# Kernel optimization log

Measured on AMD Instinct MI355X. Metric: run time of the kernel, lower is better.

The kernel has to match this reference:

```python
import jax, jax.numpy as jnp
import numpy as np

B, H, W = 8, 56, 56
DIM = 384
NH = 8
HD = DIM // NH          # 48, also the depthwise-conv channel count
WS = 14
HID = 4 * DIM           # mlp hidden
EPS = 1e-5              # torch nn.LayerNorm default
SCALE = HD ** -0.5


def ln(x, w, b):
    m = jnp.mean(x, axis=-1, keepdims=True)
    v = jnp.var(x, axis=-1, keepdims=True)
    return (x - m) * jax.lax.rsqrt(v + EPS) * w + b


def dwconv3x3(x, w):
    # x: [N,H,W,C], w: [3,3,1,C] depthwise (groups=C), stride 1, pad 1, no bias
    return jax.lax.conv_general_dilated(
        x, w, window_strides=(1, 1), padding=((1, 1), (1, 1)),
        dimension_numbers=('NHWC', 'HWIO', 'NHWC'),
        feature_group_count=x.shape[-1])


def rel_table(rel_pos, size):
    # rel_pos: [2*size-1, HD] -> [size, size, HD] via relative coords (stride 1, q==k size)
    idx = jnp.arange(size)[:, None] - jnp.arange(size)[None, :] + (size - 1)
    return rel_pos[idx]


def win_part(x, ws):
    # [N,H,W,C] -> [N*nWh*nWw, ws, ws, C]  (H,W divisible by ws here)
    N, Hh, Ww, C = x.shape
    x = x.reshape(N, Hh // ws, ws, Ww // ws, ws, C)
    return x.transpose(0, 1, 3, 2, 4, 5).reshape(-1, ws, ws, C)


def win_unpart(x, ws, Hh, Ww):
    nW = (Hh // ws) * (Ww // ws)
    N = x.shape[0] // nW
    x = x.reshape(N, Hh // ws, Ww // ws, ws, ws, -1)
    return x.transpose(0, 1, 3, 2, 4, 5).reshape(N, Hh, Ww, -1)


def _forward(x1, x2, norm1_w, norm1_b, qkv_w, qkv_b,
             poolq_w, poolk_w, poolv_w,
             nq_w, nq_b, nk_w, nk_b, nv_w, nv_b,
             rel_h, rel_w, proj_w, proj_b,
             norm2_w, norm2_b, fc1_w, fc1_b, fc2_w, fc2_b):
    # ---- F(x1): MultiScaleAttention(norm1(x1)) ----
    xn = ln(x1, norm1_w, norm1_b)
    qkv = (xn @ qkv_w + qkv_b).reshape(B, H, W, 3, NH, HD)
    qkv = qkv.transpose(3, 0, 4, 1, 2, 5).reshape(3, B * NH, H, W, HD)
    q = ln(dwconv3x3(qkv[0], poolq_w), nq_w, nq_b)
    k = ln(dwconv3x3(qkv[1], poolk_w), nk_w, nk_b)
    v = ln(dwconv3x3(qkv[2], poolv_w), nv_w, nv_b)
    ori_q = q
    qw = win_part(q, WS).reshape(-1, WS * WS, HD)   # [Bw, 196, 48]
    kw = win_part(k, WS).reshape(-1, WS * WS, HD)
    vw = win_part(v, WS).reshape(-1, WS * WS, HD)
    attn = jnp.einsum('bqc,bkc->bqk', qw * SCALE, kw)
    # decomposed relative position bias
    Rh = rel_table(rel_h, WS)                       # [14,14,48]
    Rw = rel_table(rel_w, WS)
    rq = qw.reshape(-1, WS, WS, HD)
    bh = jnp.einsum('bhwc,hkc->bhwk', rq, Rh)
    bw = jnp.einsum('bhwc,wkc->bhwk', rq, Rw)
    attn = (attn.reshape(-1, WS, WS, WS, WS)
            + bh[:, :, :, :, None] + bw[:, :, :, None, :]).reshape(-1, WS * WS, WS * WS)
    attn = jax.nn.softmax(attn, axis=-1)
    o = jnp.einsum('bqk,bkc->bqc', attn, vw).reshape(-1, WS, WS, HD)
    o = win_unpart(o, WS, H, W)
    o = o + ori_q                                    # residual pooling
    o = o.reshape(B, NH, H, W, HD).transpose(0, 2, 3, 1, 4).reshape(B, H, W, DIM)
    f = o @ proj_w + proj_b
    y1 = x1 + f
    # ---- G(y1): Mlp(norm2(y1)) ----
    yn = ln(y1, norm2_w, norm2_b)
    g = jax.nn.gelu(yn @ fc1_w + fc1_b, approximate=False) @ fc2_w + fc2_b
    y2 = x2 + g
    return y1, y2


def setup_inputs() -> dict:
    key = jax.random.key(0)
    ks = jax.random.split(key, 32)
    p = lambda i, shape, s: jax.random.normal(ks[i], shape, jnp.float32) * s
    return {
        'x1': jax.random.normal(ks[0], (B, H, W, DIM), jnp.float32),
        'x2': jax.random.normal(ks[1], (B, H, W, DIM), jnp.float32),
        'norm1_w': jnp.ones((DIM,), jnp.float32),
        'norm1_b': jnp.zeros((DIM,), jnp.float32),
        'qkv_w': p(2, (DIM, 3 * DIM), 0.02),
        'qkv_b': jnp.zeros((3 * DIM,), jnp.float32),
        'poolq_w': p(3, (3, 3, 1, HD), 0.1),
        'poolk_w': p(4, (3, 3, 1, HD), 0.1),
        'poolv_w': p(5, (3, 3, 1, HD), 0.1),
        'nq_w': jnp.ones((HD,), jnp.float32), 'nq_b': jnp.zeros((HD,), jnp.float32),
        'nk_w': jnp.ones((HD,), jnp.float32), 'nk_b': jnp.zeros((HD,), jnp.float32),
        'nv_w': jnp.ones((HD,), jnp.float32), 'nv_b': jnp.zeros((HD,), jnp.float32),
        'rel_h': p(6, (2 * WS - 1, HD), 0.02),
        'rel_w': p(7, (2 * WS - 1, HD), 0.02),
        'proj_w': p(8, (DIM, DIM), 0.02),
        'proj_b': jnp.zeros((DIM,), jnp.float32),
        'norm2_w': jnp.ones((DIM,), jnp.float32),
        'norm2_b': jnp.zeros((DIM,), jnp.float32),
        'fc1_w': p(9, (DIM, HID), 0.02),
        'fc1_b': jnp.zeros((HID,), jnp.float32),
        'fc2_w': p(10, (HID, DIM), 0.02),
        'fc2_b': jnp.zeros((DIM,), jnp.float32),
    }


def reference(x1, x2, norm1_w, norm1_b, qkv_w, qkv_b,
              poolq_w, poolk_w, poolv_w,
              nq_w, nq_b, nk_w, nk_b, nv_w, nv_b,
              rel_h, rel_w, proj_w, proj_b,
              norm2_w, norm2_b, fc1_w, fc1_b, fc2_w, fc2_b):
    return _forward(x1, x2, norm1_w, norm1_b, qkv_w, qkv_b,
                    poolq_w, poolk_w, poolv_w,
                    nq_w, nq_b, nk_w, nk_b, nv_w, nv_b,
                    rel_h, rel_w, proj_w, proj_b,
                    norm2_w, norm2_b, fc1_w, fc1_b, fc2_w, fc2_b)
```

## Files before the change

kernel.cpp:

```cpp
#include <hip/hip_runtime.h>
#include <hip/hip_bf16.h>

typedef unsigned short u16;
typedef unsigned int u32;

#define DEVI __device__ __forceinline__

constexpr int BB = 8, HHc = 56, WWc = 56, DIMC = 384, NHC = 8, HDC = 48, WSZ = 14;
constexpr int NTOK = BB * HHc * WWc;
constexpr int HIDC = 4 * DIMC;
constexpr float EPSF = 1e-5f;
constexpr float SCALEF = 0.14433756729740643f;

typedef short bf16x8 __attribute__((ext_vector_type(8)));
typedef float f32x4 __attribute__((ext_vector_type(4)));

DEVI float b2f(u16 u) { u32 x = ((u32)u) << 16; float f; __builtin_memcpy(&f, &x, 4); return f; }
DEVI float uasf(u32 x) { float f; __builtin_memcpy(&f, &x, 4); return f; }
DEVI u16 f2b(float f) {
  u32 x; __builtin_memcpy(&x, &f, 4);
  u32 r = (x >> 16) & 1u; x += 0x7fffu + r;
  return (u16)(x >> 16);
}

DEVI float wred_sum(float v) {
  #pragma unroll
  for (int o = 32; o; o >>= 1) v += __shfl_xor(v, o);
  return v;
}

#define GLOAD_LDS16(g, l) __builtin_amdgcn_global_load_lds( \
    (const __attribute__((address_space(1))) u32*)(g), \
    (__attribute__((address_space(3))) u32*)(l), 16, 0, 0)

__global__ __launch_bounds__(256)
void wcvt_kernel(const float* __restrict__ in, u16* __restrict__ out, int K, int N) {
  __shared__ float t[32][33];
  int bk = blockIdx.x * 32, bn = blockIdx.y * 32;
  int tx = threadIdx.x & 31, ty = threadIdx.x >> 5;
  #pragma unroll
  for (int i = 0; i < 32; i += 8)
    t[ty + i][tx] = in[(size_t)(bk + ty + i) * N + bn + tx];
  __syncthreads();
  #pragma unroll
  for (int i = 0; i < 32; i += 8)
    out[(size_t)(bn + ty + i) * K + bk + tx] = f2b(t[tx][ty + i]);
}

__global__ __launch_bounds__(256)
void ln384_kernel(const float* __restrict__ x, const float* __restrict__ w,
                  const float* __restrict__ b, u16* __restrict__ out) {
  int wave = threadIdx.x >> 6, lane = threadIdx.x & 63;
  int tok = blockIdx.x * 4 + wave;
  if (tok >= NTOK) return;
  const float* xr = x + (size_t)tok * DIMC;
  float v[6]; float s = 0.f, ss = 0.f;
  #pragma unroll
  for (int i = 0; i < 6; ++i) {
    v[i] = xr[lane + i * 64];
    s += v[i]; ss += v[i] * v[i];
  }
  s = wred_sum(s); ss = wred_sum(ss);
  float mean = s * (1.f / 384.f);
  float var = ss * (1.f / 384.f) - mean * mean;
  float inv = rsqrtf(var + EPSF);
  #pragma unroll
  for (int i = 0; i < 6; ++i) {
    int c = lane + i * 64;
    out[(size_t)(c >> 5) * (NTOK * 32) + (size_t)tok * 32 + (c & 31)] =
        f2b((v[i] - mean) * inv * w[c] + b[c]);
  }
}

template<int MODE>
__global__ __launch_bounds__(256)
void mgemm_kernel(const u16* __restrict__ A, const u16* __restrict__ Wt,
                  const float* __restrict__ bias, const float* __restrict__ res,
                  void* __restrict__ outv, int M, int N, int K) {
  __shared__ __attribute__((aligned(16))) u16 As[3][128 * 32];
  __shared__ __attribute__((aligned(16))) u16 Bs[3][128 * 32];
  int tid = threadIdx.x;
  int wave = tid >> 6, lane = tid & 63;
  int wr = wave >> 1, wc = wave & 1;
  int bm0 = blockIdx.x * 128, bn0 = blockIdx.y * 128;
  int lrow = lane >> 2;
  int slot = (lane & 3) ^ ((lane >> 3) & 3);
  const size_t slab = (size_t)M * 32;
  const u16* ag0 = A + (size_t)(bm0 + wave * 32 + lrow) * 32 + slot * 8;
  const u16* ag1 = ag0 + 16 * 32;
  const u16* bg0 = Wt + (size_t)(bn0 + wave * 32 + lrow) * K + slot * 8;
  const u16* bg1 = bg0 + (size_t)16 * K;
  int q4 = lane >> 4, r16 = lane & 15;
  int rslot = (q4 ^ ((r16 >> 1) & 3)) * 8;
  int aoff = (wr * 64 + r16) * 32 + rslot;
  int boff = (wc * 64 + r16) * 32 + rslot;
  f32x4 acc[4][4] = {};
  int nk = K >> 5;
  {
    u16* a0 = As[0] + wave * 1024; u16* b0 = Bs[0] + wave * 1024;
    GLOAD_LDS16(ag0, a0);              GLOAD_LDS16(ag1, a0 + 512);
    GLOAD_LDS16(bg0, b0);              GLOAD_LDS16(bg1, b0 + 512);
    u16* a1 = As[1] + wave * 1024; u16* b1 = Bs[1] + wave * 1024;
    GLOAD_LDS16(ag0 + slab, a1);       GLOAD_LDS16(ag1 + slab, a1 + 512);
    GLOAD_LDS16(bg0 + 32, b1);         GLOAD_LDS16(bg1 + 32, b1 + 512);
  }
  int cur = 0, pf = 2;
  for (int t = 0; t < nk; ++t) {
    if (t + 2 < nk) {
      int k0 = (t + 2) << 5;
      u16* a0 = As[pf] + wave * 1024; u16* b0 = Bs[pf] + wave * 1024;
      GLOAD_LDS16(ag0 + (size_t)(t + 2) * slab, a0);
      GLOAD_LDS16(ag1 + (size_t)(t + 2) * slab, a0 + 512);
      GLOAD_LDS16(bg0 + k0, b0);  GLOAD_LDS16(bg1 + k0, b0 + 512);
      asm volatile("s_waitcnt vmcnt(8)" ::: "memory");
    } else if (t + 1 < nk) {
      asm volatile("s_waitcnt vmcnt(4)" ::: "memory");
    } else {
      asm volatile("s_waitcnt vmcnt(0)" ::: "memory");
    }
    __builtin_amdgcn_s_barrier();
    const u16* ar = As[cur] + aoff;
    const u16* br = Bs[cur] + boff;
    bf16x8 af[4], bf[4];
    #pragma unroll
    for (int f = 0; f < 4; ++f) {
      af[f] = *reinterpret_cast<const bf16x8*>(ar + f * 512);
      bf[f] = *reinterpret_cast<const bf16x8*>(br + f * 512);
    }
    #pragma unroll
    for (int fm = 0; fm < 4; ++fm)
      #pragma unroll
      for (int fn = 0; fn < 4; ++fn)
        acc[fm][fn] = __builtin_amdgcn_mfma_f32_16x16x32_bf16(af[fm], bf[fn], acc[fm][fn], 0, 0, 0);
    asm volatile("s_waitcnt lgkmcnt(0)" ::: "memory");
    __builtin_amdgcn_s_barrier();
    cur = (cur == 2) ? 0 : cur + 1;
    pf  = (pf  == 2) ? 0 : pf  + 1;
  }
  int c0 = bn0 + wc * 64 + r16;
  int r0 = bm0 + wr * 64 + q4 * 4;
  #pragma unroll
  for (int fm = 0; fm < 4; ++fm) {
    #pragma unroll
    for (int fn = 0; fn < 4; ++fn) {
      int c = c0 + fn * 16;
      float bsv = bias[c];
      #pragma unroll
      for (int j = 0; j < 4; ++j) {
        int r = r0 + fm * 16 + j;
        float v = acc[fm][fn][j] + bsv;
        if constexpr (MODE == 0) {
          u16* out = (u16*)outv;
          int s = c / DIMC; int rem = c - s * DIMC;
          int nh = rem / HDC; int ch = rem - nh * HDC;
          int b = r / 3136; int hw = r - b * 3136;
          out[(((size_t)(s * 64 + b * 8 + nh)) * 3136 + hw) * 48 + ch] = f2b(v);
        } else if constexpr (MODE == 1) {
          float* out = (float*)outv;
          size_t idx = (size_t)r * N + c;
          out[idx] = v + res[idx];
        } else {
          u16* out = (u16*)outv;
          out[(size_t)(c >> 5) * M * 32 + (size_t)r * 32 + (c & 31)] =
              f2b(0.5f * v * (1.0f + erff(v * 0.70710678118654752440f)));
        }
      }
    }
  }
}

__global__ __launch_bounds__(256)
void convln_kernel(const u16* __restrict__ qkv,
                   const float* __restrict__ wq, const float* __restrict__ wk, const float* __restrict__ wv,
                   const float* __restrict__ gq, const float* __restrict__ bq,
                   const float* __restrict__ gk, const float* __restrict__ bk,
                   const float* __restrict__ gv, const float* __restrict__ bv,
                   u16* __restrict__ out) {
  __shared__ __attribute__((aligned(16))) float wsm[432];
  __shared__ __attribute__((aligned(16))) float gsm[48];
  __shared__ __attribute__((aligned(16))) float bsm[48];
  int tid = threadIdx.x;
  int sb = blockIdx.y;
  int s = sb >> 6;
  const float* wgt = (s == 0) ? wq : ((s == 1) ? wk : wv);
  const float* gam = (s == 0) ? gq : ((s == 1) ? gk : gv);
  const float* bet = (s == 0) ? bq : ((s == 1) ? bk : bv);
  for (int i = tid; i < 432; i += 256) wsm[i] = wgt[i];
  if (tid < 48) { gsm[tid] = gam[tid]; bsm[tid] = bet[tid]; }
  __syncthreads();
  int hw = blockIdx.x * 256 + tid;
  if (hw >= 3136) return;
  int h = hw / 56, w = hw - h * 56;
  const u16* img = qkv + (size_t)sb * (3136 * 48);
  float acc[48];
  #pragma unroll
  for (int c = 0; c < 48; ++c) acc[c] = 0.f;
  #pragma unroll
  for (int dy = -1; dy <= 1; ++dy) {
    int hh = h + dy;
    if ((unsigned)hh >= 56u) continue;
    #pragma unroll
    for (int dx = -1; dx <= 1; ++dx) {
      int ww = w + dx;
      if ((unsigned)ww >= 56u) continue;
      const uint4* p = reinterpret_cast<const uint4*>(img + (size_t)(hh * 56 + ww) * 48);
      const float4* wr = reinterpret_cast<const float4*>(wsm + ((dy + 1) * 3 + (dx + 1)) * 48);
      #pragma unroll
      for (int g = 0; g < 6; ++g) {
        uint4 v = p[g];
        float4 w0 = wr[g * 2], w1 = wr[g * 2 + 1];
        acc[g * 8 + 0] += uasf(v.x << 16)          * w0.x;
        acc[g * 8 + 1] += uasf(v.x & 0xFFFF0000u)  * w0.y;
        acc[g * 8 + 2] += uasf(v.y << 16)          * w0.z;
        acc[g * 8 + 3] += uasf(v.y & 0xFFFF0000u)  * w0.w;
        acc[g * 8 + 4] += uasf(v.z << 16)          * w1.x;
        acc[g * 8 + 5] += uasf(v.z & 0xFFFF0000u)  * w1.y;
        acc[g * 8 + 6] += uasf(v.w << 16)          * w1.z;
        acc[g * 8 + 7] += uasf(v.w & 0xFFFF0000u)  * w1.w;
      }
    }
  }
  float sum = 0.f, ssq = 0.f;
  #pragma unroll
  for (int c = 0; c < 48; ++c) { sum += acc[c]; ssq += acc[c] * acc[c]; }
  float mean = sum * (1.f / 48.f);
  float var = ssq * (1.f / 48.f) - mean * mean;
  float inv = rsqrtf(var + EPSF);
  u16* op = out + ((size_t)sb * 3136 + hw) * 48;
  #pragma unroll
  for (int g = 0; g < 6; ++g) {
    const float4 gm0 = *reinterpret_cast<const float4*>(gsm + g * 8);
    const float4 gm1 = *reinterpret_cast<const float4*>(gsm + g * 8 + 4);
    const float4 bt0 = *reinterpret_cast<const float4*>(bsm + g * 8);
    const float4 bt1 = *reinterpret_cast<const float4*>(bsm + g * 8 + 4);
    uint4 ov;
    u32 a0 = f2b((acc[g * 8 + 0] - mean) * inv * gm0.x + bt0.x);
    u32 a1 = f2b((acc[g * 8 + 1] - mean) * inv * gm0.y + bt0.y);
    u32 a2 = f2b((acc[g * 8 + 2] - mean) * inv * gm0.z + bt0.z);
    u32 a3 = f2b((acc[g * 8 + 3] - mean) * inv * gm0.w + bt0.w);
    u32 a4 = f2b((acc[g * 8 + 4] - mean) * inv * gm1.x + bt1.x);
    u32 a5 = f2b((acc[g * 8 + 5] - mean) * inv * gm1.y + bt1.y);
    u32 a6 = f2b((acc[g * 8 + 6] - mean) * inv * gm1.z + bt1.z);
    u32 a7 = f2b((acc[g * 8 + 7] - mean) * inv * gm1.w + bt1.w);
    ov.x = a0 | (a1 << 16);
    ov.y = a2 | (a3 << 16);
    ov.z = a4 | (a5 << 16);
    ov.w = a6 | (a7 << 16);
    *reinterpret_cast<uint4*>(op + g * 8) = ov;
  }
}

#define MFMA16(a, b, c) __builtin_amdgcn_mfma_f32_16x16x32_bf16((a), (b), (c), 0, 0, 0)
constexpr int LDP = 224;
constexpr int LDK = 104;
constexpr int LDV = 228;
__global__ __launch_bounds__(512, 1)
void attn_kernel(const u16* __restrict__ qkvc, const float* __restrict__ rel_h,
                 const float* __restrict__ rel_w, u16* __restrict__ obuf) {
  __shared__ __attribute__((aligned(16))) u16 KL[208 * LDK];
  __shared__ __attribute__((aligned(16))) u16 VT[48 * LDV];
  __shared__ __attribute__((aligned(16))) u16 QE[208 * 56];
  __shared__ __attribute__((aligned(16))) u16 PB[8 * 16 * LDP];

  int wid = blockIdx.x;
  int bnh = wid >> 4, wrem = wid & 15, wh = wrem >> 2, wwn = wrem & 3;
  int tid = threadIdx.x;
  int wave = tid >> 6, lane = tid & 63;
  int q4 = lane >> 4, r16 = lane & 15;

  { u32* z;
    z = (u32*)KL; for (int i = tid; i < 208 * LDK / 2; i += 512) z[i] = 0;
    z = (u32*)VT; for (int i = tid; i < 48 * LDV / 2; i += 512) z[i] = 0;
    z = (u32*)PB; for (int i = tid; i < 64 * 72 / 2; i += 512) z[i] = 0;
  }
  __syncthreads();
  size_t qbase = (size_t)bnh * 3136 * 48;
  size_t kbase = ((size_t)(64 + bnh) * 3136) * 48;
  size_t vbase = ((size_t)(128 + bnh) * 3136) * 48;
  for (int i = tid; i < 196 * 12; i += 512) {
    int r = i / 12, c4 = (i - r * 12) * 4;
    int h = wh * 14 + r / 14, w = wwn * 14 + r % 14;
    size_t g = (size_t)(h * 56 + w) * 48 + c4;
    ushort4 kv = *reinterpret_cast<const ushort4*>(qkvc + kbase + g);
    kv.x = f2b(b2f(kv.x) * SCALEF); kv.y = f2b(b2f(kv.y) * SCALEF);
    kv.z = f2b(b2f(kv.z) * SCALEF); kv.w = f2b(b2f(kv.w) * SCALEF);
    *reinterpret_cast<ushort4*>(KL + r * LDK + c4) = kv;
    ushort4 vv = *reinterpret_cast<const ushort4*>(qkvc + vbase + g);
    VT[(c4 + 0) * LDV + r] = vv.x; VT[(c4 + 1) * LDV + r] = vv.y;
    VT[(c4 + 2) * LDV + r] = vv.z; VT[(c4 + 3) * LDV + r] = vv.w;
  }
  for (int r = tid; r < 208; r += 512) {
    if (r < 196) {
      KL[r * LDK + 48 + r / 14] = 0x3F80;
      KL[r * LDK + 62 + r % 14] = 0x3F80;
    } else {
      KL[r * LDK + 76] = 0x3F80;
    }
  }
  for (int i = tid; i < 54 * 48; i += 512) {
    int r = i / 48, c = i - r * 48;
    float v = (r < 27) ? rel_h[r * 48 + c] : rel_w[(r - 27) * 48 + c];
    PB[r * 72 + c] = f2b(v);
  }
  __syncthreads();
  for (int mf = wave; mf < 13; mf += 8) {
    int qrow = mf * 16 + r16; int qc = qrow < 196 ? qrow : 195;
    int hq = wh * 14 + qc / 14, wq = wwn * 14 + qc % 14;
    const u16* qpg = qkvc + qbase + (size_t)(hq * 56 + wq) * 48;
    bf16x8 af0 = *reinterpret_cast<const bf16x8*>(qpg + q4 * 8);
    bf16x8 af1 = {0, 0, 0, 0, 0, 0, 0, 0};
    if (q4 < 2) af1 = *reinterpret_cast<const bf16x8*>(qpg + 32 + q4 * 8);
    #pragma unroll
    for (int nf = 0; nf < 4; ++nf) {
      bf16x8 b0 = *reinterpret_cast<const bf16x8*>(PB + (nf * 16 + r16) * 72 + q4 * 8);
      bf16x8 b1 = *reinterpret_cast<const bf16x8*>(PB + (nf * 16 + r16) * 72 + 32 + q4 * 8);
      f32x4 acc = {};
      acc = MFMA16(af0, b0, acc);
      acc = MFMA16(af1, b1, acc);
      int col = nf * 16 + r16;
      if (col < 54) {
        #pragma unroll
        for (int j = 0; j < 4; ++j)
          QE[(mf * 16 + q4 * 4 + j) * 56 + col] = f2b(acc[j]);
      }
    }
  }
  __syncthreads();
  u16 bhv[14], bwv[14];
  {
    int t = tid;
    if (t < 208) {
      int qc = t < 196 ? t : 195;
      int qh = qc / 14, qw = qc - qh * 14;
      const u16* src = QE + t * 56;
      #pragma unroll
      for (int z = 0; z < 14; ++z) {
        bhv[z] = src[qh + 13 - z];
        bwv[z] = src[27 + qw + 13 - z];
      }
    }
  }
  __syncthreads();
  {
    int t = tid;
    if (t < 208) {
      u16* dst = QE + t * 56;
      #pragma unroll
      for (int z = 0; z < 14; ++z) { dst[z] = bhv[z]; dst[14 + z] = bwv[z]; }
      dst[28] = f2b(-30000.0f);
      #pragma unroll
      for (int z = 29; z < 56; ++z) dst[z] = 0;
    }
  }
  u16* Pw = PB + wave * 16 * LDP;
  for (int i = lane; i < 16 * 16; i += 64) {
    int r = i >> 4;
    Pw[r * LDP + ((208 + (i & 15)) ^ (((r >> 2) & 3) << 3))] = 0;
  }
  __syncthreads();
  int bI = bnh >> 3, nhI = bnh & 7;
  for (int mf = wave; mf < 13; mf += 8) {
    int qrow = mf * 16 + r16; int qc = qrow < 196 ? qrow : 195;
    int hq = wh * 14 + qc / 14, wq = wwn * 14 + qc % 14;
    const u16* qpg = qkvc + qbase + (size_t)(hq * 56 + wq) * 48;
    const u16* qe = QE + qrow * 56;
    bf16x8 af0 = *reinterpret_cast<const bf16x8*>(qpg + q4 * 8);
    bf16x8 af1;
    if (q4 < 2) af1 = *reinterpret_cast<const bf16x8*>(qpg + 32 + q4 * 8);
    else        af1 = *reinterpret_cast<const bf16x8*>(qe + (q4 - 2) * 8);
    bf16x8 af2 = *reinterpret_cast<const bf16x8*>(qe + 16 + q4 * 8);
    f32x4 s[13];
    #pragma unroll
    for (int nf = 0; nf < 13; ++nf) {
      const u16* kr = KL + (nf * 16 + r16) * LDK;
      bf16x8 b0 = *reinterpret_cast<const bf16x8*>(kr + q4 * 8);
      bf16x8 b1 = *reinterpret_cast<const bf16x8*>(kr + 32 + q4 * 8);
      bf16x8 b2 = *reinterpret_cast<const bf16x8*>(kr + 64 + q4 * 8);
      f32x4 a = {};
      a = MFMA16(af0, b0, a);
      a = MFMA16(af1, b1, a);
      a = MFMA16(af2, b2, a);
      s[nf] = a;
    }
    int rowb = mf * 16 + q4 * 4;
    float mrow[4], den[4];
    #pragma unroll
    for (int j = 0; j < 4; ++j) {
      float mm = s[0][j];
      #pragma unroll
      for (int nf = 1; nf < 13; ++nf) mm = fmaxf(mm, s[nf][j]);
      #pragma unroll
      for (int off = 1; off < 16; off <<= 1) mm = fmaxf(mm, __shfl_xor(mm, off));
      mrow[j] = mm; den[j] = 0.f;
    }
    #pragma unroll
    for (int nf = 0; nf < 13; ++nf) {
      #pragma unroll
      for (int j = 0; j < 4; ++j) {
        float p = __expf(s[nf][j] - mrow[j]);
        den[j] += p;
        Pw[(q4 * 4 + j) * LDP + (((nf * 16 + r16) ^ (q4 << 3)))] = f2b(p);
      }
    }
    #pragma unroll
    for (int j = 0; j < 4; ++j)
      #pragma unroll
      for (int off = 1; off < 16; off <<= 1) den[j] += __shfl_xor(den[j], off);
    f32x4 o[3] = {};
    #pragma unroll
    for (int ks = 0; ks < 7; ++ks) {
      bf16x8 ap = *reinterpret_cast<const bf16x8*>(
          Pw + r16 * LDP + ((ks * 32 + q4 * 8) ^ (((r16 >> 2) & 3) << 3)));
      #pragma unroll
      for (int nf3 = 0; nf3 < 3; ++nf3) {
        bf16x8 bv = *reinterpret_cast<const bf16x8*>(VT + (nf3 * 16 + r16) * LDV + ks * 32 + q4 * 8);
        o[nf3] = MFMA16(ap, bv, o[nf3]);
      }
    }
    #pragma unroll
    for (int j = 0; j < 4; ++j) {
      int row = rowb + j;
      if (row < 196) {
        float rden = 1.f / den[j];
        int rh = row / 14;
        int h = wh * 14 + rh, w = wwn * 14 + row - rh * 14;
        int tok = (bI * 56 + h) * 56 + w;
        const u16* qg = qkvc + qbase + (size_t)(h * 56 + w) * 48;
        #pragma unroll
        for (int nf3 = 0; nf3 < 3; ++nf3) {
          int col = nf3 * 16 + r16;
          int cg = nhI * 48 + col;
          obuf[(size_t)(cg >> 5) * (NTOK * 32) + (size_t)tok * 32 + (cg & 31)] =
              f2b(o[nf3][j] * rden + b2f(qg[col]));
        }
      }
    }
  }
}

extern "C" void kernel_launch(void* const* d_in, const int* in_sizes, int n_in,
                              void* d_out, int out_size, void* d_ws, size_t ws_size,
                              hipStream_t stream) {
  const float* x1      = (const float*)d_in[0];
  const float* x2      = (const float*)d_in[1];
  const float* norm1_w = (const float*)d_in[2];
  const float* norm1_b = (const float*)d_in[3];
  const float* qkv_w   = (const float*)d_in[4];
  const float* qkv_b   = (const float*)d_in[5];
  const float* poolq_w = (const float*)d_in[6];
  const float* poolk_w = (const float*)d_in[7];
  const float* poolv_w = (const float*)d_in[8];
  const float* nq_w    = (const float*)d_in[9];
  const float* nq_b    = (const float*)d_in[10];
  const float* nk_w    = (const float*)d_in[11];
  const float* nk_b    = (const float*)d_in[12];
  const float* nv_w    = (const float*)d_in[13];
  const float* nv_b    = (const float*)d_in[14];
  const float* rel_h   = (const float*)d_in[15];
  const float* rel_w   = (const float*)d_in[16];
  const float* proj_w  = (const float*)d_in[17];
  const float* proj_b  = (const float*)d_in[18];
  const float* norm2_w = (const float*)d_in[19];
  const float* norm2_b = (const float*)d_in[20];
  const float* fc1_w   = (const float*)d_in[21];
  const float* fc1_b   = (const float*)d_in[22];
  const float* fc2_w   = (const float*)d_in[23];
  const float* fc2_b   = (const float*)d_in[24];

  u16* ws      = (u16*)d_ws;
  u16* qkv     = ws;
  u16* xn      = ws + 28901376;
  u16* qkvc    = ws + 28901376;
  u16* obuf    = ws;
  u16* h1      = ws;
  u16* yn      = ws + 48168960;
  u16* qkv_wt  = ws + 38535168;
  u16* proj_wt = ws + 9633792;
  u16* fc1_wt  = ws + 38535168;
  u16* fc2_wt  = ws + 39124992;
  float* y1 = (float*)d_out;
  float* y2 = y1 + 9633792;

  wcvt_kernel<<<dim3(12, 36), 256, 0, stream>>>(qkv_w, qkv_wt, 384, 1152);
  ln384_kernel<<<NTOK / 4, 256, 0, stream>>>(x1, norm1_w, norm1_b, xn);
  mgemm_kernel<0><<<dim3(196, 9), 256, 0, stream>>>(xn, qkv_wt, qkv_b, nullptr, qkv, NTOK, 1152, 384);
  convln_kernel<<<dim3(13, 192), 256, 0, stream>>>(qkv, poolq_w, poolk_w, poolv_w,
                                                   nq_w, nq_b, nk_w, nk_b, nv_w, nv_b, qkvc);
  wcvt_kernel<<<dim3(12, 12), 256, 0, stream>>>(proj_w, proj_wt, 384, 384);
  attn_kernel<<<1024, 512, 0, stream>>>(qkvc, rel_h, rel_w, obuf);
  wcvt_kernel<<<dim3(12, 48), 256, 0, stream>>>(fc1_w, fc1_wt, 384, 1536);
  wcvt_kernel<<<dim3(48, 12), 256, 0, stream>>>(fc2_w, fc2_wt, 1536, 384);
  mgemm_kernel<1><<<dim3(196, 3), 256, 0, stream>>>(obuf, proj_wt, proj_b, x1, y1, NTOK, 384, 384);
  ln384_kernel<<<NTOK / 4, 256, 0, stream>>>(y1, norm2_w, norm2_b, yn);
  mgemm_kernel<2><<<dim3(196, 12), 256, 0, stream>>>(yn, fc1_wt, fc1_b, nullptr, h1, NTOK, 1536, 384);
  mgemm_kernel<1><<<dim3(196, 3), 256, 0, stream>>>(h1, fc2_wt, fc2_b, x2, y2, NTOK, 384, 1536);
}
```

Before: 372.4 us.

## Template GEMM on N tile width and switch to double-buffered LDS pipeline

Adds a BN template parameter so the two N=384 GEMMs (proj, fc2) use 128x64 tiles with twice as many blocks, improving occupancy and CU coverage for the smaller output. It also replaces the triple-buffered, two-ahead prefetch with a double-buffered, one-ahead prefetch, cutting LDS use per block. The trade-off is less prefetch depth, which may expose more global load latency, and a lower MFMA-to-load ratio in the 64-wide variant.

```diff
diff --git a/kernel.cpp b/kernel.cpp
--- a/kernel.cpp
+++ b/kernel.cpp
@@ -72,77 +72,78 @@
   }
 }
 
-template<int MODE>
+template<int MODE, int BN>
 __global__ __launch_bounds__(256)
 void mgemm_kernel(const u16* __restrict__ A, const u16* __restrict__ Wt,
                   const float* __restrict__ bias, const float* __restrict__ res,
                   void* __restrict__ outv, int M, int N, int K) {
-  __shared__ __attribute__((aligned(16))) u16 As[3][128 * 32];
-  __shared__ __attribute__((aligned(16))) u16 Bs[3][128 * 32];
+  constexpr int FN = BN / 32;
+  __shared__ __attribute__((aligned(16))) u16 As[2][128 * 32];
+  __shared__ __attribute__((aligned(16))) u16 Bs[2][BN * 32];
   int tid = threadIdx.x;
   int wave = tid >> 6, lane = tid & 63;
   int wr = wave >> 1, wc = wave & 1;
-  int bm0 = blockIdx.x * 128, bn0 = blockIdx.y * 128;
+  int bm0 = blockIdx.x * 128, bn0 = blockIdx.y * BN;
   int lrow = lane >> 2;
   int slot = (lane & 3) ^ ((lane >> 3) & 3);
   const size_t slab = (size_t)M * 32;
   const u16* ag0 = A + (size_t)(bm0 + wave * 32 + lrow) * 32 + slot * 8;
   const u16* ag1 = ag0 + 16 * 32;
-  const u16* bg0 = Wt + (size_t)(bn0 + wave * 32 + lrow) * K + slot * 8;
+  const u16* bg0 = Wt + (size_t)(bn0 + wave * (BN / 4) + lrow) * K + slot * 8;
   const u16* bg1 = bg0 + (size_t)16 * K;
   int q4 = lane >> 4, r16 = lane & 15;
   int rslot = (q4 ^ ((r16 >> 1) & 3)) * 8;
   int aoff = (wr * 64 + r16) * 32 + rslot;
-  int boff = (wc * 64 + r16) * 32 + rslot;
-  f32x4 acc[4][4] = {};
+  int boff = (wc * (BN / 2) + r16) * 32 + rslot;
+  f32x4 acc[4][FN] = {};
   int nk = K >> 5;
   {
-    u16* a0 = As[0] + wave * 1024; u16* b0 = Bs[0] + wave * 1024;
-    GLOAD_LDS16(ag0, a0);              GLOAD_LDS16(ag1, a0 + 512);
-    GLOAD_LDS16(bg0, b0);              GLOAD_LDS16(bg1, b0 + 512);
-    u16* a1 = As[1] + wave * 1024; u16* b1 = Bs[1] + wave * 1024;
-    GLOAD_LDS16(ag0 + slab, a1);       GLOAD_LDS16(ag1 + slab, a1 + 512);
-    GLOAD_LDS16(bg0 + 32, b1);         GLOAD_LDS16(bg1 + 32, b1 + 512);
-  }
-  int cur = 0, pf = 2;
+    u16* a0 = As[0] + wave * 1024;
+    u16* b0 = Bs[0] + wave * (BN / 4) * 32;
+    GLOAD_LDS16(ag0, a0);  GLOAD_LDS16(ag1, a0 + 512);
+    GLOAD_LDS16(bg0, b0);
+    if constexpr (BN == 128) GLOAD_LDS16(bg1, b0 + 512);
+  }
+  int cur = 0;
   for (int t = 0; t < nk; ++t) {
-    if (t + 2 < nk) {
-      int k0 = (t + 2) << 5;
-      u16* a0 = As[pf] + wave * 1024; u16* b0 = Bs[pf] + wave * 1024;
-      GLOAD_LDS16(ag0 + (size_t)(t + 2) * slab, a0);
-      GLOAD_LDS16(ag1 + (size_t)(t + 2) * slab, a0 + 512);
-      GLOAD_LDS16(bg0 + k0, b0);  GLOAD_LDS16(bg1 + k0, b0 + 512);
-      asm volatile("s_waitcnt vmcnt(8)" ::: "memory");
-    } else if (t + 1 < nk) {
-      asm volatile("s_waitcnt vmcnt(4)" ::: "memory");
+    if (t + 1 < nk) {
+      int k0 = (t + 1) << 5;
+      u16* a0 = As[cur ^ 1] + wave * 1024;
+      u16* b0 = Bs[cur ^ 1] + wave * (BN / 4) * 32;
+      GLOAD_LDS16(ag0 + (size_t)(t + 1) * slab, a0);
+      GLOAD_LDS16(ag1 + (size_t)(t + 1) * slab, a0 + 512);
+      GLOAD_LDS16(bg0 + k0, b0);
+      if constexpr (BN == 128) GLOAD_LDS16(bg1 + k0, b0 + 512);
+      if constexpr (BN == 128) asm volatile("s_waitcnt vmcnt(4)" ::: "memory");
+      else                     asm volatile("s_waitcnt vmcnt(3)" ::: "memory");
     } else {
       asm volatile("s_waitcnt vmcnt(0)" ::: "memory");
     }
     __builtin_amdgcn_s_barrier();
     const u16* ar = As[cur] + aoff;
     const u16* br = Bs[cur] + boff;
-    bf16x8 af[4], bf[4];
-    #pragma unroll
-    for (int f = 0; f < 4; ++f) {
+    bf16x8 af[4], bf[FN];
+    #pragma unroll
+    for (int f = 0; f < 4; ++f)
       af[f] = *reinterpret_cast<const bf16x8*>(ar + f * 512);
+    #pragma unroll
+    for (int f = 0; f < FN; ++f)
       bf[f] = *reinterpret_cast<const bf16x8*>(br + f * 512);
-    }
     #pragma unroll
     for (int fm = 0; fm < 4; ++fm)
       #pragma unroll
-      for (int fn = 0; fn < 4; ++fn)
+      for (int fn = 0; fn < FN; ++fn)
         acc[fm][fn] = __builtin_amdgcn_mfma_f32_16x16x32_bf16(af[fm], bf[fn], acc[fm][fn], 0, 0, 0);
     asm volatile("s_waitcnt lgkmcnt(0)" ::: "memory");
     __builtin_amdgcn_s_barrier();
-    cur = (cur == 2) ? 0 : cur + 1;
-    pf  = (pf  == 2) ? 0 : pf  + 1;
-  }
-  int c0 = bn0 + wc * 64 + r16;
+    cur ^= 1;
+  }
+  int c0 = bn0 + wc * (BN / 2) + r16;
   int r0 = bm0 + wr * 64 + q4 * 4;
   #pragma unroll
   for (int fm = 0; fm < 4; ++fm) {
     #pragma unroll
-    for (int fn = 0; fn < 4; ++fn) {
+    for (int fn = 0; fn < FN; ++fn) {
       int c = c0 + fn * 16;
       float bsv = bias[c];
       #pragma unroll
@@ -483,15 +484,15 @@
 
   wcvt_kernel<<<dim3(12, 36), 256, 0, stream>>>(qkv_w, qkv_wt, 384, 1152);
   ln384_kernel<<<NTOK / 4, 256, 0, stream>>>(x1, norm1_w, norm1_b, xn);
-  mgemm_kernel<0><<<dim3(196, 9), 256, 0, stream>>>(xn, qkv_wt, qkv_b, nullptr, qkv, NTOK, 1152, 384);
+  mgemm_kernel<0, 128><<<dim3(196, 9), 256, 0, stream>>>(xn, qkv_wt, qkv_b, nullptr, qkv, NTOK, 1152, 384);
   convln_kernel<<<dim3(13, 192), 256, 0, stream>>>(qkv, poolq_w, poolk_w, poolv_w,
                                                    nq_w, nq_b, nk_w, nk_b, nv_w, nv_b, qkvc);
   wcvt_kernel<<<dim3(12, 12), 256, 0, stream>>>(proj_w, proj_wt, 384, 384);
   attn_kernel<<<1024, 512, 0, stream>>>(qkvc, rel_h, rel_w, obuf);
   wcvt_kernel<<<dim3(12, 48), 256, 0, stream>>>(fc1_w, fc1_wt, 384, 1536);
   wcvt_kernel<<<dim3(48, 12), 256, 0, stream>>>(fc2_w, fc2_wt, 1536, 384);
-  mgemm_kernel<1><<<dim3(196, 3), 256, 0, stream>>>(obuf, proj_wt, proj_b, x1, y1, NTOK, 384, 384);
+  mgemm_kernel<1, 64><<<dim3(196, 6), 256, 0, stream>>>(obuf, proj_wt, proj_b, x1, y1, NTOK, 384, 384);
   ln384_kernel<<<NTOK / 4, 256, 0, stream>>>(y1, norm2_w, norm2_b, yn);
-  mgemm_kernel<2><<<dim3(196, 12), 256, 0, stream>>>(yn, fc1_wt, fc1_b, nullptr, h1, NTOK, 1536, 384);
-  mgemm_kernel<1><<<dim3(196, 3), 256, 0, stream>>>(h1, fc2_wt, fc2_b, x2, y2, NTOK, 384, 1536);
-}
+  mgemm_kernel<2, 128><<<dim3(196, 12), 256, 0, stream>>>(yn, fc1_wt, fc1_b, nullptr, h1, NTOK, 1536, 384);
+  mgemm_kernel<1, 64><<<dim3(196, 6), 256, 0, stream>>>(h1, fc2_wt, fc2_b, x2, y2, NTOK, 384, 1536);
+}
```

Result: faster. 361.4 us (-3.0%).

## Replace 4-wave 128x128 GEMM with single-wave 64x64 GEMM, B in registers

Applied to the files above, without the earlier changes.

Replaces the 256-thread 128x128-tile GEMM with a 64-thread single-wave kernel that computes a 64x64 tile. Only A is staged in LDS, through a 4-deep async ring. B fragments are loaded straight from global memory into double-buffered registers. This removes the block-level barriers and the B LDS traffic, and launches far more, smaller blocks for load balancing. The cost is less data reuse per tile: each A and B element is fetched from global/L2 more often, and direct global B loads may add latency.

```diff
diff --git a/kernel.cpp b/kernel.cpp
--- a/kernel.cpp
+++ b/kernel.cpp
@@ -32,6 +32,8 @@
 #define GLOAD_LDS16(g, l) __builtin_amdgcn_global_load_lds( \
     (const __attribute__((address_space(1))) u32*)(g), \
     (__attribute__((address_space(3))) u32*)(l), 16, 0, 0)
+
+#define MFMA16(a, b, c) __builtin_amdgcn_mfma_f32_16x16x32_bf16((a), (b), (c), 0, 0, 0)
 
 __global__ __launch_bounds__(256)
 void wcvt_kernel(const float* __restrict__ in, u16* __restrict__ out, int K, int N) {
@@ -73,81 +75,76 @@
 }
 
 template<int MODE>
-__global__ __launch_bounds__(256)
-void mgemm_kernel(const u16* __restrict__ A, const u16* __restrict__ Wt,
+__global__ __launch_bounds__(64)
+void wgemm_kernel(const u16* __restrict__ A, const u16* __restrict__ Wt,
                   const float* __restrict__ bias, const float* __restrict__ res,
                   void* __restrict__ outv, int M, int N, int K) {
-  __shared__ __attribute__((aligned(16))) u16 As[3][128 * 32];
-  __shared__ __attribute__((aligned(16))) u16 Bs[3][128 * 32];
-  int tid = threadIdx.x;
-  int wave = tid >> 6, lane = tid & 63;
-  int wr = wave >> 1, wc = wave & 1;
-  int bm0 = blockIdx.x * 128, bn0 = blockIdx.y * 128;
+  __shared__ __attribute__((aligned(16))) u16 As[4][64 * 32];
+  int lane = threadIdx.x;
+  int q4 = lane >> 4, r16 = lane & 15;
+  int bm0 = blockIdx.y * 64, bn0 = blockIdx.x * 64;
   int lrow = lane >> 2;
   int slot = (lane & 3) ^ ((lane >> 3) & 3);
   const size_t slab = (size_t)M * 32;
-  const u16* ag0 = A + (size_t)(bm0 + wave * 32 + lrow) * 32 + slot * 8;
-  const u16* ag1 = ag0 + 16 * 32;
-  const u16* bg0 = Wt + (size_t)(bn0 + wave * 32 + lrow) * K + slot * 8;
-  const u16* bg1 = bg0 + (size_t)16 * K;
-  int q4 = lane >> 4, r16 = lane & 15;
+  const u16* ag = A + (size_t)(bm0 + lrow) * 32 + slot * 8;
+  const u16* bg = Wt + (size_t)(bn0 + r16) * K + q4 * 8;
   int rslot = (q4 ^ ((r16 >> 1) & 3)) * 8;
-  int aoff = (wr * 64 + r16) * 32 + rslot;
-  int boff = (wc * 64 + r16) * 32 + rslot;
+  const int aoff = r16 * 32 + rslot;
   f32x4 acc[4][4] = {};
   int nk = K >> 5;
-  {
-    u16* a0 = As[0] + wave * 1024; u16* b0 = Bs[0] + wave * 1024;
-    GLOAD_LDS16(ag0, a0);              GLOAD_LDS16(ag1, a0 + 512);
-    GLOAD_LDS16(bg0, b0);              GLOAD_LDS16(bg1, b0 + 512);
-    u16* a1 = As[1] + wave * 1024; u16* b1 = Bs[1] + wave * 1024;
-    GLOAD_LDS16(ag0 + slab, a1);       GLOAD_LDS16(ag1 + slab, a1 + 512);
-    GLOAD_LDS16(bg0 + 32, b1);         GLOAD_LDS16(bg1 + 32, b1 + 512);
-  }
-  int cur = 0, pf = 2;
-  for (int t = 0; t < nk; ++t) {
-    if (t + 2 < nk) {
-      int k0 = (t + 2) << 5;
-      u16* a0 = As[pf] + wave * 1024; u16* b0 = Bs[pf] + wave * 1024;
-      GLOAD_LDS16(ag0 + (size_t)(t + 2) * slab, a0);
-      GLOAD_LDS16(ag1 + (size_t)(t + 2) * slab, a0 + 512);
-      GLOAD_LDS16(bg0 + k0, b0);  GLOAD_LDS16(bg1 + k0, b0 + 512);
-      asm volatile("s_waitcnt vmcnt(8)" ::: "memory");
-    } else if (t + 1 < nk) {
-      asm volatile("s_waitcnt vmcnt(4)" ::: "memory");
-    } else {
-      asm volatile("s_waitcnt vmcnt(0)" ::: "memory");
-    }
-    __builtin_amdgcn_s_barrier();
-    const u16* ar = As[cur] + aoff;
-    const u16* br = Bs[cur] + boff;
-    bf16x8 af[4], bf[4];
-    #pragma unroll
-    for (int f = 0; f < 4; ++f) {
-      af[f] = *reinterpret_cast<const bf16x8*>(ar + f * 512);
-      bf[f] = *reinterpret_cast<const bf16x8*>(br + f * 512);
-    }
-    #pragma unroll
-    for (int fm = 0; fm < 4; ++fm)
-      #pragma unroll
-      for (int fn = 0; fn < 4; ++fn)
-        acc[fm][fn] = __builtin_amdgcn_mfma_f32_16x16x32_bf16(af[fm], bf[fn], acc[fm][fn], 0, 0, 0);
-    asm volatile("s_waitcnt lgkmcnt(0)" ::: "memory");
-    __builtin_amdgcn_s_barrier();
-    cur = (cur == 2) ? 0 : cur + 1;
-    pf  = (pf  == 2) ? 0 : pf  + 1;
-  }
-  int c0 = bn0 + wc * 64 + r16;
-  int r0 = bm0 + wr * 64 + q4 * 4;
+  bf16x8 bA[4], bB[4];
+  #pragma unroll
+  for (int fn = 0; fn < 4; ++fn)
+    bA[fn] = *reinterpret_cast<const bf16x8*>(bg + (size_t)fn * 16 * K);
+  #pragma unroll
+  for (int i = 0; i < 3; ++i)
+    #pragma unroll
+    for (int r = 0; r < 4; ++r)
+      GLOAD_LDS16(ag + (size_t)i * slab + r * 16 * 32, As[i] + r * 16 * 32);
+
+#define WG_STEP(TT, BU, BL)                                                    \
+  {                                                                            \
+    int tt = (TT);                                                             \
+    if (tt + 1 < nk) {                                                         \
+      _Pragma("unroll")                                                        \
+      for (int fn = 0; fn < 4; ++fn)                                           \
+        BL[fn] = *reinterpret_cast<const bf16x8*>(                             \
+            bg + (size_t)fn * 16 * K + (tt + 1) * 32);                         \
+    }                                                                          \
+    if (tt + 3 < nk) {                                                         \
+      _Pragma("unroll")                                                        \
+      for (int r = 0; r < 4; ++r)                                              \
+        GLOAD_LDS16(ag + (size_t)(tt + 3) * slab + r * 16 * 32,                \
+                    As[(tt + 3) & 3] + r * 16 * 32);                           \
+      asm volatile("s_waitcnt vmcnt(12)" ::: "memory");                        \
+    } else {                                                                   \
+      asm volatile("s_waitcnt vmcnt(0)" ::: "memory");                         \
+    }                                                                          \
+    const u16* ar = As[tt & 3] + aoff;                                         \
+    _Pragma("unroll")                                                          \
+    for (int fm = 0; fm < 4; ++fm) {                                           \
+      bf16x8 af = *reinterpret_cast<const bf16x8*>(ar + fm * 16 * 32);         \
+      _Pragma("unroll")                                                        \
+      for (int fn = 0; fn < 4; ++fn)                                           \
+        acc[fm][fn] = MFMA16(af, BU[fn], acc[fm][fn]);                         \
+    }                                                                          \
+    asm volatile("s_waitcnt lgkmcnt(0)" ::: "memory");                         \
+  }
+
+  for (int t = 0; t < nk; t += 2) {
+    WG_STEP(t,     bA, bB);
+    WG_STEP(t + 1, bB, bA);
+  }
+#undef WG_STEP
   #pragma unroll
   for (int fm = 0; fm < 4; ++fm) {
     #pragma unroll
     for (int fn = 0; fn < 4; ++fn) {
-      int c = c0 + fn * 16;
+      int c = bn0 + fn * 16 + r16;
       float bsv = bias[c];
       #pragma unroll
       for (int j = 0; j < 4; ++j) {
-        int r = r0 + fm * 16 + j;
+        int r = bm0 + fm * 16 + q4 * 4 + j;
         float v = acc[fm][fn][j] + bsv;
         if constexpr (MODE == 0) {
           u16* out = (u16*)outv;
@@ -250,7 +247,6 @@
   }
 }
 
-#define MFMA16(a, b, c) __builtin_amdgcn_mfma_f32_16x16x32_bf16((a), (b), (c), 0, 0, 0)
 constexpr int LDP = 224;
 constexpr int LDK = 104;
 constexpr int LDV = 228;
@@ -483,15 +479,15 @@
 
   wcvt_kernel<<<dim3(12, 36), 256, 0, stream>>>(qkv_w, qkv_wt, 384, 1152);
   ln384_kernel<<<NTOK / 4, 256, 0, stream>>>(x1, norm1_w, norm1_b, xn);
-  mgemm_kernel<0><<<dim3(196, 9), 256, 0, stream>>>(xn, qkv_wt, qkv_b, nullptr, qkv, NTOK, 1152, 384);
+  wgemm_kernel<0><<<dim3(18, 392), 64, 0, stream>>>(xn, qkv_wt, qkv_b, nullptr, qkv, NTOK, 1152, 384);
   convln_kernel<<<dim3(13, 192), 256, 0, stream>>>(qkv, poolq_w, poolk_w, poolv_w,
                                                    nq_w, nq_b, nk_w, nk_b, nv_w, nv_b, qkvc);
   wcvt_kernel<<<dim3(12, 12), 256, 0, stream>>>(proj_w, proj_wt, 384, 384);
   attn_kernel<<<1024, 512, 0, stream>>>(qkvc, rel_h, rel_w, obuf);
   wcvt_kernel<<<dim3(12, 48), 256, 0, stream>>>(fc1_w, fc1_wt, 384, 1536);
   wcvt_kernel<<<dim3(48, 12), 256, 0, stream>>>(fc2_w, fc2_wt, 1536, 384);
-  mgemm_kernel<1><<<dim3(196, 3), 256, 0, stream>>>(obuf, proj_wt, proj_b, x1, y1, NTOK, 384, 384);
+  wgemm_kernel<1><<<dim3(6, 392), 64, 0, stream>>>(obuf, proj_wt, proj_b, x1, y1, NTOK, 384, 384);
   ln384_kernel<<<NTOK / 4, 256, 0, stream>>>(y1, norm2_w, norm2_b, yn);
-  mgemm_kernel<2><<<dim3(196, 12), 256, 0, stream>>>(yn, fc1_wt, fc1_b, nullptr, h1, NTOK, 1536, 384);
-  mgemm_kernel<1><<<dim3(196, 3), 256, 0, stream>>>(h1, fc2_wt, fc2_b, x2, y2, NTOK, 384, 1536);
-}
+  wgemm_kernel<2><<<dim3(24, 392), 64, 0, stream>>>(yn, fc1_wt, fc1_b, nullptr, h1, NTOK, 1536, 384);
+  wgemm_kernel<1><<<dim3(6, 392), 64, 0, stream>>>(h1, fc2_wt, fc2_b, x2, y2, NTOK, 384, 1536);
+}
```

Measured after the change: 446.2 us. 19.8% more time.
